# Kernel optimization log

Hardware: AMD Instinct MI355X
Metric: run time of the kernel (lower is better)

The kernel has to match this reference:

```python
import jax, jax.numpy as jnp
import numpy as np

T, B, H, L = 2048, 2048, 8, 4  # seq_len, batch, hidden_size, num_layers


def setup_inputs() -> dict:
    key = jax.random.key(0)
    ks = jax.random.split(key, 8)
    s = 1.0 / np.sqrt(H)  # torch nn.RNN/Linear default uniform(-1/sqrt(H), 1/sqrt(H))
    u = lambda k, shape: jax.random.uniform(k, shape, jnp.float32, -s, s)
    return {
        "x": jax.random.normal(ks[0], (T, B, 1), jnp.float32),
        "initial_h": jnp.zeros((L, B, H), jnp.float32),
        "w_ih0": u(ks[1], (H, 1)),       # layer 0 input weight
        "w_ih": u(ks[2], (L - 1, H, H)),  # layers 1..3 input weights
        "w_hh": u(ks[3], (L, H, H)),
        "b_ih": u(ks[4], (L, H)),
        "b_hh": u(ks[5], (L, H)),
        "w_lin": u(ks[6], (1, H)),
        "b_lin": u(ks[7], (1,)),
    }


def _rnn_forward(x, initial_h, w_ih0, w_ih, w_hh, b_ih, b_hh, w_lin, b_lin):
    # Stacked vanilla tanh RNN, time-major: h_t^l = tanh(W_ih x + b_ih + W_hh h + b_hh)
    def step(h_all, x_t):  # h_all: (L, B, H), x_t: (B, 1)
        h_new0 = jnp.tanh(x_t @ w_ih0.T + b_ih[0] + h_all[0] @ w_hh[0].T + b_hh[0])
        hs = [h_new0]
        for l in range(1, L):  # fixed small layer loop
            hs.append(jnp.tanh(hs[-1] @ w_ih[l - 1].T + b_ih[l]
                               + h_all[l] @ w_hh[l].T + b_hh[l]))
        return jnp.stack(hs), hs[-1]

    _, out = jax.lax.scan(step, initial_h, x)  # out: (T, B, H) top-layer outputs
    # Faithful to the torch code: initial_h.dim()==3 -> out[:, -1, :] on a
    # TIME-MAJOR tensor, i.e. last BATCH element for every timestep -> (T, H)
    out_sel = out[:, -1, :]
    return out_sel @ w_lin.T + b_lin  # (T, 1)


def reference(x, initial_h, w_ih0, w_ih, w_hh, b_ih, b_hh, w_lin, b_lin):
    return _rnn_forward(x, initial_h, w_ih0, w_ih, w_hh, b_ih, b_hh, w_lin, b_lin)
```

## Files before the change

### kernel.cpp

```cpp
#include <hip/hip_runtime.h>

#define T_LEN 2048
#define B_SZ  2048
#define H_SZ  8
#define SKEW  5
#define WARM  20
#define XS_N  2080

template<int CTRL>
__device__ __forceinline__ float rot_dpp(float v) {
    return __int_as_float(
        __builtin_amdgcn_update_dpp(0, __float_as_int(v), CTRL, 0xF, 0xF, false));
}

__global__ __launch_bounds__(64, 1)
void rnn_fasm(const float* __restrict__ x,
              const float* __restrict__ h0_in,
              const float* __restrict__ w_ih0,
              const float* __restrict__ w_ih,
              const float* __restrict__ w_hh,
              const float* __restrict__ b_ih,
              const float* __restrict__ b_hh,
              const float* __restrict__ w_lin,
              const float* __restrict__ b_lin,
              float* __restrict__ out)
{
    __shared__ __align__(16) float xs[XS_N];

    const int lane = threadIdx.x;
    const int u    = lane & 7;
    const int l    = lane >> 4;
    const bool grB = ((lane >> 3) & 1);
    const int lp   = (l + 3) & 3;
    const int bidx = (((lp << 4) | 8 | u)) << 2;

    for (int i = lane; i < XS_N; i += 64) xs[i] = 0.0f;
    __syncthreads();
    for (int i = lane; i < T_LEN; i += 64) xs[i] = x[(size_t)i * B_SZ + (B_SZ - 1)];
    __syncthreads();

    int rot1 = __builtin_amdgcn_update_dpp(0, lane, 0x121, 0xF, 0xF, false);
    const bool plus = ((rot1 & 15) == ((lane + 1) & 15));

    const float C   = 2.0f * 1.4426950408889634f;
    const float m2C = -2.0f * C;

    float whh_rs = 0.0f, wih_rs = 0.0f, wlin_rs = 0.0f;
    #pragma unroll
    for (int j = 0; j < 8; ++j) {
        whh_rs += w_hh[(l * H_SZ + u) * H_SZ + j];
        if (l > 0) wih_rs += w_ih[((l - 1) * H_SZ + u) * H_SZ + j];
        wlin_rs += w_lin[j];
    }
    const float bl_tot = wlin_rs + b_lin[0];

    float wsel[8];
    #pragma unroll
    for (int s = 0; s < 8; ++s) {
        int j = plus ? ((u + s) & 7) : ((u - s) & 7);
        float whh2  = m2C * w_hh[(l * H_SZ + u) * H_SZ + j];
        float wexp2 = (l < 3) ? m2C * w_ih[(l * H_SZ + u) * H_SZ + j]
                              : -2.0f * w_lin[j];
        wsel[s] = grB ? wexp2 : whh2;
    }
    const float tbase = (grB && l == 3) ? bl_tot : 0.0f;
    const float xconst_a = C * (b_ih[l * H_SZ + u] + b_hh[l * H_SZ + u]
                                + whh_rs + ((l > 0) ? wih_rs : 0.0f));
    const float wx2p    = (!grB && l == 0) ? C * w_ih0[u] : 0.0f;
    const float xconstp = grB ? tbase : xconst_a;
    const float selp    = (grB || l == 0) ? 0.0f : 1.0f;

    float r = __builtin_fmaf(-0.5f, h0_in[((size_t)l * B_SZ + (B_SZ - 1)) * H_SZ + u], 0.5f);

    float ip0 = 0.0f, ip1 = 0.0f, ip2 = 0.0f, ip3 = 0.0f;

    auto tick = [&](float& ip_slot, float base, float xv_next, float& t_out) -> float {
        float c0 = base, c1, S, e, t, rn;
        asm("s_nop 0\n\t"
            "v_fma_f32      %[c0], %[w0], %[r], %[c0]\n\t"
            "v_mul_f32_dpp  %[c1], %[r], %[w4] row_ror:4 row_mask:0xf bank_mask:0xf\n\t"
            "v_fmac_f32_dpp %[c0], %[r], %[w1] row_ror:1 row_mask:0xf bank_mask:0xf\n\t"
            "v_fmac_f32_dpp %[c1], %[r], %[w5] row_ror:5 row_mask:0xf bank_mask:0xf\n\t"
            "v_fmac_f32_dpp %[c0], %[r], %[w2] row_ror:2 row_mask:0xf bank_mask:0xf\n\t"
            "v_fmac_f32_dpp %[c1], %[r], %[w6] row_ror:6 row_mask:0xf bank_mask:0xf\n\t"
            "v_fmac_f32_dpp %[c0], %[r], %[w3] row_ror:3 row_mask:0xf bank_mask:0xf\n\t"
            "v_fmac_f32_dpp %[c1], %[r], %[w7] row_ror:7 row_mask:0xf bank_mask:0xf\n\t"
            "v_add_f32      %[S], %[c0], %[c1]\n\t"
            "v_exp_f32      %[e], %[S]\n\t"
            "v_fma_f32      %[t], %[wx], %[xv], %[xc]\n\t"
            "s_nop 0\n\t"
            "v_mov_b32_dpp  %[e], %[e] row_ror:8 row_mask:0xf bank_mask:0xc\n\t"
            "v_add_f32      %[e], 1.0, %[e]\n\t"
            "v_rcp_f32      %[rn], %[e]"
            : [c0]"+v"(c0), [c1]"=&v"(c1), [S]"=&v"(S), [e]"=&v"(e),
              [t]"=&v"(t), [rn]"=&v"(rn)
            : [r]"v"(r), [w0]"v"(wsel[0]), [w1]"v"(wsel[1]), [w2]"v"(wsel[2]),
              [w3]"v"(wsel[3]), [w4]"v"(wsel[4]), [w5]"v"(wsel[5]),
              [w6]"v"(wsel[6]), [w7]"v"(wsel[7]),
              [wx]"v"(wx2p), [xv]"v"(xv_next), [xc]"v"(xconstp));
        ip_slot = __int_as_float(__builtin_amdgcn_ds_bpermute(bidx, __float_as_int(S)));
        t_out = t;
        return rn;
    };

    float baseA = __builtin_fmaf(wx2p, xs[0], xconstp);
    float baseB = 0.0f;
    #pragma unroll
    for (int k = 0; k < WARM; ++k) {
        float rn, t;
        if      ((k & 3) == 0) { rn = tick(ip0, baseA, xs[k + 1], t); baseB = __builtin_fmaf(selp, ip1, t); }
        else if ((k & 3) == 1) { rn = tick(ip1, baseB, xs[k + 1], t); baseA = __builtin_fmaf(selp, ip2, t); }
        else if ((k & 3) == 2) { rn = tick(ip2, baseA, xs[k + 1], t); baseB = __builtin_fmaf(selp, ip3, t); }
        else                   { rn = tick(ip3, baseB, xs[k + 1], t); baseA = __builtin_fmaf(selp, ip0, t); }
        r = (k >= SKEW * l) ? rn : r;
    }
    float ov_carry = ip0;

    const float4* xsv = (const float4*)xs;
    float4 xq  = xsv[5];
    float4 xq2 = xsv[6];
    for (int kb = WARM; kb <= 2060; kb += 8) {
        float4 xn1 = xsv[(kb >> 2) + 2];
        float4 xn2 = xsv[(kb >> 2) + 3];
        float o0 = ov_carry, o1, o2, o3, o4, o5, o6, o7, t;
        r = tick(ip0, baseA, xq.y,  t); o1 = ip1; baseB = __builtin_fmaf(selp, ip1, t);
        r = tick(ip1, baseB, xq.z,  t); o2 = ip2; baseA = __builtin_fmaf(selp, ip2, t);
        r = tick(ip2, baseA, xq.w,  t); o3 = ip3; baseB = __builtin_fmaf(selp, ip3, t);
        r = tick(ip3, baseB, xq2.x, t); o4 = ip0; baseA = __builtin_fmaf(selp, ip0, t);
        r = tick(ip0, baseA, xq2.y, t); o5 = ip1; baseB = __builtin_fmaf(selp, ip1, t);
        r = tick(ip1, baseB, xq2.z, t); o6 = ip2; baseA = __builtin_fmaf(selp, ip2, t);
        r = tick(ip2, baseA, xq2.w, t); o7 = ip3; baseB = __builtin_fmaf(selp, ip3, t);
        r = tick(ip3, baseB, xn1.x, t); ov_carry = ip0; baseA = __builtin_fmaf(selp, ip0, t);
        if (lane == 0) {
            *(float4*)(out + (kb - WARM))     = make_float4(o0, o1, o2, o3);
            *(float4*)(out + (kb - WARM) + 4) = make_float4(o4, o5, o6, o7);
        }
        xq = xn1; xq2 = xn2;
    }
}

extern "C" void kernel_launch(void* const* d_in, const int* in_sizes, int n_in,
                              void* d_out, int out_size, void* d_ws, size_t ws_size,
                              hipStream_t stream) {
    const float* x     = (const float*)d_in[0];
    const float* h0    = (const float*)d_in[1];
    const float* w_ih0 = (const float*)d_in[2];
    const float* w_ih  = (const float*)d_in[3];
    const float* w_hh  = (const float*)d_in[4];
    const float* b_ih  = (const float*)d_in[5];
    const float* b_hh  = (const float*)d_in[6];
    const float* w_lin = (const float*)d_in[7];
    const float* b_lin = (const float*)d_in[8];
    float* out = (float*)d_out;

    rnn_fasm<<<dim3(1), dim3(64), 0, stream>>>(
        x, h0, w_ih0, w_ih, w_hh, b_ih, b_hh, w_lin, b_lin, out);
}
```

Before: 177.4 us.

## Compute recurrent and export matvecs in every lane with split accumulators

Before, the 16-lane rows were split into two half-groups: one computed the recurrent matvec, the other the export/projection matvec, and a row_ror:8 DPP move shared the exp result between them. Now every lane computes both matvecs itself. Each matvec uses four independent accumulators joined by an add tree, which shortens the serial dependency chain ahead of exp/rcp. The export dot product is placed after the exp so it can overlap transcendental latency. The cost is twice as many VALU instructions per tick and more live registers in a single-wave, latency-bound kernel.

```diff
diff --git a/kernel.cpp b/kernel.cpp
--- a/kernel.cpp
+++ b/kernel.cpp
@@ -6,12 +6,6 @@
 #define SKEW  5
 #define WARM  20
 #define XS_N  2080
-
-template<int CTRL>
-__device__ __forceinline__ float rot_dpp(float v) {
-    return __int_as_float(
-        __builtin_amdgcn_update_dpp(0, __float_as_int(v), CTRL, 0xF, 0xF, false));
-}
 
 __global__ __launch_bounds__(64, 1)
 void rnn_fasm(const float* __restrict__ x,
@@ -54,52 +48,62 @@
     }
     const float bl_tot = wlin_rs + b_lin[0];
 
-    float wsel[8];
+    float wown[8], wexp[8];
     #pragma unroll
     for (int s = 0; s < 8; ++s) {
         int j = plus ? ((u + s) & 7) : ((u - s) & 7);
-        float whh2  = m2C * w_hh[(l * H_SZ + u) * H_SZ + j];
-        float wexp2 = (l < 3) ? m2C * w_ih[(l * H_SZ + u) * H_SZ + j]
-                              : -2.0f * w_lin[j];
-        wsel[s] = grB ? wexp2 : whh2;
+        wown[s] = m2C * w_hh[(l * H_SZ + u) * H_SZ + j];
+        wexp[s] = (l < 3) ? m2C * w_ih[(l * H_SZ + u) * H_SZ + j]
+                          : -2.0f * w_lin[j];
     }
-    const float tbase = (grB && l == 3) ? bl_tot : 0.0f;
-    const float xconst_a = C * (b_ih[l * H_SZ + u] + b_hh[l * H_SZ + u]
-                                + whh_rs + ((l > 0) ? wih_rs : 0.0f));
-    const float wx2p    = (!grB && l == 0) ? C * w_ih0[u] : 0.0f;
-    const float xconstp = grB ? tbase : xconst_a;
-    const float selp    = (grB || l == 0) ? 0.0f : 1.0f;
+    const float tb = (grB && l == 3) ? bl_tot : 0.0f;
+    const float xconstp = C * (b_ih[l * H_SZ + u] + b_hh[l * H_SZ + u]
+                               + whh_rs + ((l > 0) ? wih_rs : 0.0f));
+    const float wx2p    = (l == 0) ? C * w_ih0[u] : 0.0f;
+    const float selp    = (l == 0) ? 0.0f : 1.0f;
 
     float r = __builtin_fmaf(-0.5f, h0_in[((size_t)l * B_SZ + (B_SZ - 1)) * H_SZ + u], 0.5f);
 
     float ip0 = 0.0f, ip1 = 0.0f, ip2 = 0.0f, ip3 = 0.0f;
 
     auto tick = [&](float& ip_slot, float base, float xv_next, float& t_out) -> float {
-        float c0 = base, c1, S, e, t, rn;
-        asm("s_nop 0\n\t"
-            "v_fma_f32      %[c0], %[w0], %[r], %[c0]\n\t"
-            "v_mul_f32_dpp  %[c1], %[r], %[w4] row_ror:4 row_mask:0xf bank_mask:0xf\n\t"
+        float c0 = base, c1, c2, c3, d0, d1, d2, d3, e, rn;
+        asm("v_fma_f32      %[c0], %[w0], %[r], %[c0]\n\t"
+            "v_mul_f32_dpp  %[c1], %[r], %[w2] row_ror:2 row_mask:0xf bank_mask:0xf\n\t"
+            "v_mul_f32_dpp  %[c2], %[r], %[w4] row_ror:4 row_mask:0xf bank_mask:0xf\n\t"
+            "v_mul_f32_dpp  %[c3], %[r], %[w6] row_ror:6 row_mask:0xf bank_mask:0xf\n\t"
             "v_fmac_f32_dpp %[c0], %[r], %[w1] row_ror:1 row_mask:0xf bank_mask:0xf\n\t"
-            "v_fmac_f32_dpp %[c1], %[r], %[w5] row_ror:5 row_mask:0xf bank_mask:0xf\n\t"
-            "v_fmac_f32_dpp %[c0], %[r], %[w2] row_ror:2 row_mask:0xf bank_mask:0xf\n\t"
-            "v_fmac_f32_dpp %[c1], %[r], %[w6] row_ror:6 row_mask:0xf bank_mask:0xf\n\t"
-            "v_fmac_f32_dpp %[c0], %[r], %[w3] row_ror:3 row_mask:0xf bank_mask:0xf\n\t"
-            "v_fmac_f32_dpp %[c1], %[r], %[w7] row_ror:7 row_mask:0xf bank_mask:0xf\n\t"
-            "v_add_f32      %[S], %[c0], %[c1]\n\t"
-            "v_exp_f32      %[e], %[S]\n\t"
-            "v_fma_f32      %[t], %[wx], %[xv], %[xc]\n\t"
-            "s_nop 0\n\t"
-            "v_mov_b32_dpp  %[e], %[e] row_ror:8 row_mask:0xf bank_mask:0xc\n\t"
+            "v_fmac_f32_dpp %[c1], %[r], %[w3] row_ror:3 row_mask:0xf bank_mask:0xf\n\t"
+            "v_fmac_f32_dpp %[c2], %[r], %[w5] row_ror:5 row_mask:0xf bank_mask:0xf\n\t"
+            "v_fmac_f32_dpp %[c3], %[r], %[w7] row_ror:7 row_mask:0xf bank_mask:0xf\n\t"
+            "v_add_f32      %[c0], %[c0], %[c1]\n\t"
+            "v_add_f32      %[c2], %[c2], %[c3]\n\t"
+            "v_add_f32      %[c0], %[c0], %[c2]\n\t"
+            "v_exp_f32      %[e], %[c0]\n\t"
+            "v_fma_f32      %[d0], %[e0], %[r], %[tb]\n\t"
+            "v_mul_f32_dpp  %[d1], %[r], %[e2] row_ror:2 row_mask:0xf bank_mask:0xf\n\t"
+            "v_mul_f32_dpp  %[d2], %[r], %[e4] row_ror:4 row_mask:0xf bank_mask:0xf\n\t"
+            "v_mul_f32_dpp  %[d3], %[r], %[e6] row_ror:6 row_mask:0xf bank_mask:0xf\n\t"
+            "v_fmac_f32_dpp %[d0], %[r], %[e1] row_ror:1 row_mask:0xf bank_mask:0xf\n\t"
+            "v_fmac_f32_dpp %[d1], %[r], %[e3] row_ror:3 row_mask:0xf bank_mask:0xf\n\t"
+            "v_fmac_f32_dpp %[d2], %[r], %[e5] row_ror:5 row_mask:0xf bank_mask:0xf\n\t"
+            "v_fmac_f32_dpp %[d3], %[r], %[e7] row_ror:7 row_mask:0xf bank_mask:0xf\n\t"
             "v_add_f32      %[e], 1.0, %[e]\n\t"
-            "v_rcp_f32      %[rn], %[e]"
-            : [c0]"+v"(c0), [c1]"=&v"(c1), [S]"=&v"(S), [e]"=&v"(e),
-              [t]"=&v"(t), [rn]"=&v"(rn)
-            : [r]"v"(r), [w0]"v"(wsel[0]), [w1]"v"(wsel[1]), [w2]"v"(wsel[2]),
-              [w3]"v"(wsel[3]), [w4]"v"(wsel[4]), [w5]"v"(wsel[5]),
-              [w6]"v"(wsel[6]), [w7]"v"(wsel[7]),
-              [wx]"v"(wx2p), [xv]"v"(xv_next), [xc]"v"(xconstp));
-        ip_slot = __int_as_float(__builtin_amdgcn_ds_bpermute(bidx, __float_as_int(S)));
-        t_out = t;
+            "v_rcp_f32      %[rn], %[e]\n\t"
+            "v_add_f32      %[d0], %[d0], %[d1]\n\t"
+            "v_add_f32      %[d2], %[d2], %[d3]\n\t"
+            "v_add_f32      %[d0], %[d0], %[d2]"
+            : [c0]"+v"(c0), [c1]"=&v"(c1), [c2]"=&v"(c2), [c3]"=&v"(c3),
+              [d0]"=&v"(d0), [d1]"=&v"(d1), [d2]"=&v"(d2), [d3]"=&v"(d3),
+              [e]"=&v"(e), [rn]"=&v"(rn)
+            : [r]"v"(r),
+              [w0]"v"(wown[0]), [w1]"v"(wown[1]), [w2]"v"(wown[2]), [w3]"v"(wown[3]),
+              [w4]"v"(wown[4]), [w5]"v"(wown[5]), [w6]"v"(wown[6]), [w7]"v"(wown[7]),
+              [e0]"v"(wexp[0]), [e1]"v"(wexp[1]), [e2]"v"(wexp[2]), [e3]"v"(wexp[3]),
+              [e4]"v"(wexp[4]), [e5]"v"(wexp[5]), [e6]"v"(wexp[6]), [e7]"v"(wexp[7]),
+              [tb]"v"(tb));
+        ip_slot = __int_as_float(__builtin_amdgcn_ds_bpermute(bidx, __float_as_int(d0)));
+        t_out = __builtin_fmaf(wx2p, xv_next, xconstp);
         return rn;
     };
 
```

Measured after the change: 218.3 us. 23.1% more time.
